# Kernel optimization log

Hardware: AMD Instinct MI355X
Metric: run time of the kernel (lower is better)

The kernel has to match this reference:

```python
import jax, jax.numpy as jnp
import numpy as np

N = 10000      # num_nodes (also input feature width per GCNConv(num_nodes, 200))
E = 320000     # num edges (avg degree 32)
H1 = 200
C = 8
N_TEST = 2000


def _gcn_norm(edge_index, edge_weight, num_nodes):
    """PyG GCNConv symmetric normalization with self-loops (fill value 1)."""
    loop = jnp.arange(num_nodes)
    row = jnp.concatenate([edge_index[0], loop])          # source nodes
    col = jnp.concatenate([edge_index[1], loop])          # target nodes
    w = jnp.concatenate([edge_weight, jnp.ones((num_nodes,), edge_weight.dtype)])
    deg = jax.ops.segment_sum(w, col, num_segments=num_nodes)
    dis = jnp.where(deg > 0, jax.lax.rsqrt(deg), 0.0)     # deg^{-1/2}, 0 for isolated
    norm = dis[row] * w * dis[col]
    return row, col, norm


def _gcn_conv(x, row, col, norm, W, b, num_nodes):
    h = x @ W                                             # linear transform first (PyG order)
    msg = h[row] * norm[:, None]                          # gather + scale
    out = jax.ops.segment_sum(msg, col, num_segments=num_nodes)  # scatter-add aggregate
    return out + b


def setup_inputs() -> dict:
    key = jax.random.key(0)
    ks = jax.random.split(key, 8)
    x = jax.random.normal(ks[0], (N, N), jnp.float32)
    edge_index = jax.random.randint(ks[1], (2, E), 0, N, dtype=jnp.int64) if jax.config.read('jax_enable_x64') else jax.random.randint(ks[1], (2, E), 0, N)
    edge_weight = jax.random.uniform(ks[2], (E,), jnp.float32)
    mask_idx = jax.random.randint(ks[3], (N_TEST,), 0, N)
    y = jax.random.randint(ks[4], (N,), 0, C)
    W1 = jax.random.normal(ks[5], (N, H1), jnp.float32) / np.sqrt(N).astype(np.float32)
    b1 = jnp.zeros((H1,), jnp.float32)
    W2 = jax.random.normal(ks[6], (H1, C), jnp.float32) / np.sqrt(H1).astype(np.float32)
    b2 = jnp.zeros((C,), jnp.float32)
    return {"x": x, "edge_index": edge_index, "edge_weight": edge_weight,
            "mask_idx": mask_idx, "y": y, "W1": W1, "b1": b1, "W2": W2, "b2": b2}


def reference(x, edge_index, edge_weight, mask_idx, y, W1, b1, W2, b2):
    row, col, norm = _gcn_norm(edge_index, edge_weight, N)
    h = _gcn_conv(x, row, col, norm, W1, b1, N)
    h = jax.nn.relu(h)
    # dropout: module run in eval mode -> identity
    h = _gcn_conv(h, row, col, norm, W2, b2, N)
    predictions = h[mask_idx]   # masked gather (mode='test')
    targets = y[mask_idx]
    return predictions, targets
```

## Files before the change

kernel.cpp:

```cpp
#include <hip/hip_runtime.h>
#include <hip/hip_bf16.h>

#define NN     10000
#define NE     320000
#define H1DIM  200
#define H1BST  208
#define NCLS   8
#define NTST   2000
#define KDIM   10000
#define KPAD   10048
#define KSPL   6
#define KSTEPS 26
#define NGEMMB 474

typedef __bf16 bf16x8 __attribute__((ext_vector_type(8)));
typedef float  f32x4  __attribute__((ext_vector_type(4)));

__device__ __forceinline__ void load_lds16(const void* g, void* l) {
  __builtin_amdgcn_global_load_lds(
      (__attribute__((address_space(1))) void*)(void*)g,
      (__attribute__((address_space(3))) void*)l, 16, 0, 0);
}


__global__ void k_prep0(float* deg, int* cnt, int* cur, int* flags,
                        const unsigned* ei, const unsigned* mk, const unsigned* yy,
                        const float* __restrict__ W1, __bf16* __restrict__ Wt) {
  __shared__ float tile[64][65];
  __shared__ int s_f[4];
  int b = blockIdx.x, t = threadIdx.x;
  if (b < 40) {
    int i = b * 256 + t;
    if (i < NN) { deg[i] = 1.0f; cnt[i] = 0; cur[i] = 0; }
    return;
  }
  if (b < 43) {
    unsigned a = 0;
    if (b == 40)      { for (int i = t; i < 2048; i += 256) a |= ei[2 * i + 1]; }
    else if (b == 41) { for (int i = t; i < 2048; i += 256) a |= yy[2 * i + 1]; }
    else              { for (int i = t; i < 900;  i += 256) a |= mk[2 * i + 1]; }
    int wid = t >> 6;
    int any = __any(a != 0) ? 1 : 0;
    if ((t & 63) == 0) s_f[wid] = any;
    __syncthreads();
    if (t == 0) {
      int f = s_f[0] | s_f[1] | s_f[2] | s_f[3];
      int idx = (b == 40) ? 0 : (b == 41) ? 2 : 1;
      flags[idx] = f;
    }
    return;
  }
  int bt = b - 43;
  int k0 = (bt % 157) * 64, n0 = (bt / 157) * 64;
  int tn = t & 63, tk = t >> 6;
  for (int r = 0; r < 64; r += 4) {
    int k = k0 + tk + r, n = n0 + tn;
    tile[tk + r][tn] = (k < KDIM && n < H1DIM) ? W1[k * H1DIM + n] : 0.f;
  }
  __syncthreads();
  for (int r = 0; r < 64; r += 4) {
    int n = n0 + tk + r, k = k0 + tn;
    if (k < KPAD && n < 256)
      Wt[(size_t)n * KPAD + k] = (__bf16)tile[tn][tk + r];
  }
}


__launch_bounds__(512, 4)
__global__ void k_gemm_cvt(const float* __restrict__ x, const __bf16* __restrict__ Wt,
                           __bf16* __restrict__ hpart,
                           const void* ei, const void* mk, const void* yy,
                           const float* __restrict__ ew, const int* __restrict__ flags,
                           int* idx32, int* mask32, int* y32, float* deg, int* cnt) {
  int t = threadIdx.x;
  if (blockIdx.x >= NGEMMB) {
    int i = (blockIdx.x - NGEMMB) * 512 + t;
    if (i < NE) {
      int v = (flags[0] == 0) ? (int)((const long long*)ei)[i] : ((const int*)ei)[i];
      idx32[i] = min(max(v, 0), NN - 1);
    } else if (i < 2 * NE) {
      int v = (flags[0] == 0) ? (int)((const long long*)ei)[i] : ((const int*)ei)[i];
      v = min(max(v, 0), NN - 1);
      idx32[i] = v;
      atomicAdd(&deg[v], ew[i - NE]);
      atomicAdd(&cnt[v], 1);
    } else if (i < 2 * NE + NTST) {
      int j = i - 2 * NE;
      int v = (flags[1] == 0) ? (int)((const long long*)mk)[j] : ((const int*)mk)[j];
      mask32[j] = min(max(v, 0), NN - 1);
    } else if (i < 2 * NE + NTST + NN) {
      int j = i - 2 * NE - NTST;
      int v = (flags[2] == 0) ? (int)((const long long*)yy)[j] : ((const int*)yy)[j];
      y32[j] = min(max(v, 0), NN - 1);
    }
    return;
  }

  __shared__ __align__(16) __bf16 As[128 * 64];
  __shared__ __align__(16) __bf16 Bs[256 * 64];
  int wv = t >> 6, lane = t & 63;
  int wm = wv >> 2, wn = wv & 3;
  int m0 = (blockIdx.x % 79) * 128;
  int split = blockIdx.x / 79;
  int kbeg = split * (KSTEPS * 64);
  int nsteps = KSTEPS + ((split == KSPL - 1) ? 1 : 0);

  f32x4 acc[4][4];
  #pragma unroll
  for (int i = 0; i < 4; ++i)
    #pragma unroll
    for (int j = 0; j < 4; ++j)
      #pragma unroll
      for (int r = 0; r < 4; ++r) acc[i][j][r] = 0.f;

  int am = t >> 2;
  int ac = t & 3;
  long arow = m0 + am; if (arow >= NN) arow = NN - 1;
  const float* aptr = x + (size_t)arow * KDIM + ac * 16;
  int ag0 = (2 * ac + 0) ^ (am & 7);
  int ag1 = (2 * ac + 1) ^ (am & 7);
  __bf16* awr0 = As + am * 64 + ag0 * 8;
  __bf16* awr1 = As + am * 64 + ag1 * 8;

  const __bf16* bsrc[4];
  __bf16* bdst[4];
  #pragma unroll
  for (int pass = 0; pass < 4; ++pass) {
    int s = pass * 512 + t;
    int brow = s >> 3, bg = s & 7;
    bsrc[pass] = Wt + (size_t)brow * KPAD + ((bg ^ (brow & 7)) * 8);
    bdst[pass] = Bs + (size_t)(pass * 512 + wv * 64) * 8;
  }

  int lrow = lane & 15;
  int lhi = lane >> 4;
  int lx7 = lane & 7;

  float4 v0, v1, v2, v3;
  {
    bool pr = (kbeg + ac * 16 + 16 <= KDIM);
    if (pr) {
      const float4* p = (const float4*)(aptr + kbeg);
      v0 = p[0]; v1 = p[1]; v2 = p[2]; v3 = p[3];
    }
  }

  for (int ks = 0; ks < nsteps; ++ks) {
    int k0 = kbeg + ks * 64;
    #pragma unroll
    for (int pass = 0; pass < 4; ++pass)
      load_lds16(bsrc[pass] + k0, bdst[pass]);
    {
      bool pr = (k0 + ac * 16 + 16 <= KDIM);
      bf16x8 bva, bvb;
      if (pr) {
        bva[0] = (__bf16)v0.x; bva[1] = (__bf16)v0.y;
        bva[2] = (__bf16)v0.z; bva[3] = (__bf16)v0.w;
        bva[4] = (__bf16)v1.x; bva[5] = (__bf16)v1.y;
        bva[6] = (__bf16)v1.z; bva[7] = (__bf16)v1.w;
        bvb[0] = (__bf16)v2.x; bvb[1] = (__bf16)v2.y;
        bvb[2] = (__bf16)v2.z; bvb[3] = (__bf16)v2.w;
        bvb[4] = (__bf16)v3.x; bvb[5] = (__bf16)v3.y;
        bvb[6] = (__bf16)v3.z; bvb[7] = (__bf16)v3.w;
      } else {
        #pragma unroll
        for (int q = 0; q < 8; ++q) { bva[q] = (__bf16)0.f; bvb[q] = (__bf16)0.f; }
      }
      *(bf16x8*)awr0 = bva;
      *(bf16x8*)awr1 = bvb;
    }
    __syncthreads();

    if (ks + 1 < nsteps) {
      int k1 = k0 + 64;
      bool pr = (k1 + ac * 16 + 16 <= KDIM);
      if (pr) {
        const float4* p = (const float4*)(aptr + k1);
        v0 = p[0]; v1 = p[1]; v2 = p[2]; v3 = p[3];
      }
    }

    #pragma unroll
    for (int kk = 0; kk < 2; ++kk) {
      int gs8 = ((kk * 4 + lhi) ^ lx7) * 8;
      bf16x8 af[4], bf[4];
      #pragma unroll
      for (int i = 0; i < 4; ++i)
        af[i] = *(const bf16x8*)&As[(wm * 64 + i * 16 + lrow) * 64 + gs8];
      #pragma unroll
      for (int j = 0; j < 4; ++j)
        bf[j] = *(const bf16x8*)&Bs[(wn * 64 + j * 16 + lrow) * 64 + gs8];
      #pragma unroll
      for (int i = 0; i < 4; ++i)
        #pragma unroll
        for (int j = 0; j < 4; ++j)
          acc[i][j] = __builtin_amdgcn_mfma_f32_16x16x32_bf16(af[i], bf[j], acc[i][j], 0, 0, 0);
    }
    __syncthreads();
  }

  __bf16* outp = hpart + (size_t)split * NN * H1BST;
  int colb = wn * 64 + (lane & 15);
  int rbase = m0 + wm * 64 + ((lane >> 4) * 4);
  #pragma unroll
  for (int i = 0; i < 4; ++i)
    #pragma unroll
    for (int j = 0; j < 4; ++j) {
      int cg = colb + j * 16;
      if (cg < H1BST) {
        #pragma unroll
        for (int r = 0; r < 4; ++r) {
          int rg = rbase + i * 16 + r;
          if (rg < NN) outp[(size_t)rg * H1BST + cg] = (__bf16)acc[i][j][r];
        }
      }
    }
}


__global__ void k_scan_red(const int* __restrict__ cnt, const float* __restrict__ deg,
                           float* dis, int* rowptr,
                           const __bf16* __restrict__ hpart, __bf16* __restrict__ h1b) {
  int t = threadIdx.x;
  if (blockIdx.x > 0) {
    int i = (blockIdx.x - 1) * 1024 + t;
    if (i < NN * 26) {
      int c = i / 26, ch = i - c * 26;
      size_t base = (size_t)c * H1BST + ch * 8;
      float s[8];
      #pragma unroll
      for (int q = 0; q < 8; ++q) s[q] = 0.f;
      #pragma unroll
      for (int sp = 0; sp < KSPL; ++sp) {
        bf16x8 v = *(const bf16x8*)(hpart + (size_t)sp * NN * H1BST + base);
        #pragma unroll
        for (int q = 0; q < 8; ++q) s[q] += (float)v[q];
      }
      bf16x8 o;
      #pragma unroll
      for (int q = 0; q < 8; ++q) o[q] = (__bf16)s[q];
      *(bf16x8*)&h1b[base] = o;
    }
    return;
  }
  __shared__ int wsum[16];
  __shared__ int carry;
  int lane = t & 63, wid = t >> 6;
  if (t == 0) carry = 0;
  __syncthreads();
  for (int base = 0; base < NN; base += 1024) {
    int idx = base + t;
    if (idx < NN) { float d = deg[idx]; dis[idx] = (d > 0.f) ? rsqrtf(d) : 0.f; }
    int v = (idx < NN) ? cnt[idx] : 0;
    int x = v;
    #pragma unroll
    for (int off = 1; off < 64; off <<= 1) {
      int y = __shfl_up(x, off);
      if (lane >= off) x += y;
    }
    if (lane == 63) wsum[wid] = x;
    __syncthreads();
    int c0 = carry;
    if (t < 16) {
      int s = wsum[t];
      #pragma unroll
      for (int off = 1; off < 16; off <<= 1) {
        int y = __shfl_up(s, off);
        if (t >= off) s += y;
      }
      wsum[t] = s;
    }
    __syncthreads();
    int woff = (wid == 0) ? 0 : wsum[wid - 1];
    if (idx < NN) rowptr[idx] = c0 + woff + x - v;
    int tot = wsum[15];
    __syncthreads();
    if (t == 0) carry = c0 + tot;
    __syncthreads();
  }
  if (t == 0) rowptr[NN] = carry;
}

__global__ void k_norm_scatter(const int* __restrict__ rows, const int* __restrict__ cols,
                               const float* __restrict__ w, const float* __restrict__ dis,
                               const int* __restrict__ rowptr, int* cur,
                               float* normv, int* eids) {
  int e = blockIdx.x * 512 + threadIdx.x;
  if (e < NE) {
    int r = rows[e], c = cols[e];
    normv[e] = dis[r] * w[e] * dis[c];
    int pos = rowptr[c] + atomicAdd(&cur[c], 1);
    eids[pos] = e;
  }
}


__global__ void k_agg1lin2(const __bf16* __restrict__ h1b, const float* __restrict__ dis,
                           const float* __restrict__ normv, const int* __restrict__ rows,
                           const int* __restrict__ rowptr, const int* __restrict__ eids,
                           const float* __restrict__ b1, const float* __restrict__ W2,
                           float* __restrict__ h2) {
  __shared__ int   s_r[512];
  __shared__ float s_n[512];
  __shared__ float s_p[4][8];
  int c = blockIdx.x;
  int t = threadIdx.x;
  int lane = t & 63, wid = t >> 6;
  int p0 = rowptr[c], len = rowptr[c + 1] - p0;
  float acc = 0.f;
  for (int base = 0; base < len; base += 512) {
    int chunk = min(512, len - base);
    for (int j = t; j < chunk; j += 256) {
      int e = eids[p0 + base + j];
      s_r[j] = rows[e];
      s_n[j] = normv[e];
    }
    __syncthreads();
    if (t < H1DIM) {
      int j = 0;
      for (; j + 4 <= chunk; j += 4) {
        float v0 = s_n[j + 0] * (float)h1b[(size_t)s_r[j + 0] * H1BST + t];
        float v1 = s_n[j + 1] * (float)h1b[(size_t)s_r[j + 1] * H1BST + t];
        float v2 = s_n[j + 2] * (float)h1b[(size_t)s_r[j + 2] * H1BST + t];
        float v3 = s_n[j + 3] * (float)h1b[(size_t)s_r[j + 3] * H1BST + t];
        acc += v0 + v1 + v2 + v3;
      }
      for (; j < chunk; ++j) acc += s_n[j] * (float)h1b[(size_t)s_r[j] * H1BST + t];
    }
    __syncthreads();
  }
  float a = 0.f;
  if (t < H1DIM) {
    float d = dis[c];
    a = acc + d * d * (float)h1b[(size_t)c * H1BST + t] + b1[t];
    a = fmaxf(a, 0.f);
  }
  float p[8];
  if (t < H1DIM) {
    float4 w2a = *(const float4*)&W2[t * 8];
    float4 w2b = *(const float4*)&W2[t * 8 + 4];
    p[0] = a * w2a.x; p[1] = a * w2a.y; p[2] = a * w2a.z; p[3] = a * w2a.w;
    p[4] = a * w2b.x; p[5] = a * w2b.y; p[6] = a * w2b.z; p[7] = a * w2b.w;
  } else {
    #pragma unroll
    for (int o = 0; o < 8; ++o) p[o] = 0.f;
  }
  #pragma unroll
  for (int s = 32; s >= 1; s >>= 1) {
    #pragma unroll
    for (int o = 0; o < 8; ++o) p[o] += __shfl_down(p[o], s);
  }
  if (lane == 0) {
    #pragma unroll
    for (int o = 0; o < 8; ++o) s_p[wid][o] = p[o];
  }
  __syncthreads();
  if (t < 8)
    h2[(size_t)c * 8 + t] = s_p[0][t] + s_p[1][t] + s_p[2][t] + s_p[3][t];
}


__global__ void k_agg2out(const float* __restrict__ h2, const float* __restrict__ dis,
                          const float* __restrict__ normv, const int* __restrict__ rows,
                          const int* __restrict__ rowptr, const int* __restrict__ eids,
                          const float* __restrict__ b2, const int* __restrict__ mask,
                          const int* __restrict__ yv, float* __restrict__ out) {
  int i = blockIdx.x * 256 + threadIdx.x;
  if (i < NTST * NCLS) {
    int r = i >> 3, o = i & 7;
    int c = mask[r];
    float d = dis[c];
    float acc = d * d * h2[c * NCLS + o];
    int p0 = rowptr[c], p1 = rowptr[c + 1];
    for (int j = p0; j < p1; ++j) {
      int e = eids[j];
      acc += normv[e] * h2[rows[e] * NCLS + o];
    }
    out[i] = acc + b2[o];
  } else if (i < NTST * NCLS + NTST) {
    int r = i - NTST * NCLS;
    out[i] = (float)yv[mask[r]];
  }
}


extern "C" void kernel_launch(void* const* d_in, const int* in_sizes, int n_in,
                              void* d_out, int out_size, void* d_ws, size_t ws_size,
                              hipStream_t stream) {
  const float* x    = (const float*)d_in[0];
  const void*  ei   = d_in[1];
  const float* ew   = (const float*)d_in[2];
  const void*  mask = d_in[3];
  const void*  y    = d_in[4];
  const float* W1   = (const float*)d_in[5];
  const float* b1   = (const float*)d_in[6];
  const float* W2   = (const float*)d_in[7];
  const float* b2   = (const float*)d_in[8];
  float* out = (float*)d_out;

  char* ws = (char*)d_ws;
  float* deg    = (float*)(ws + 0);
  float* dis    = (float*)(ws + (64 << 10));
  float* normv  = (float*)(ws + (128 << 10));
  int*   idx32  = (int*)(ws + (2 << 20));
  float* h2     = (float*)(ws + (5 << 20));
  int*   mask32 = (int*)(ws + (6 << 20));
  int*   y32    = (int*)(ws + (6 << 20) + (64 << 10));
  int*   flags  = (int*)(ws + (6 << 20) + (128 << 10));
  int*   cnt    = (int*)(ws + (6 << 20) + (256 << 10));
  int*   cur    = (int*)(ws + (6 << 20) + (384 << 10));
  int*   rowptr = (int*)(ws + (6 << 20) + (512 << 10));
  int*   eids   = (int*)(ws + (7 << 20));
  __bf16* Wt    = (__bf16*)(ws + ((size_t)9 << 20));
  __bf16* h1b   = (__bf16*)(ws + ((size_t)16 << 20));
  __bf16* hpart = (__bf16*)(ws + ((size_t)24 << 20));

  int* rows32 = idx32;
  int* cols32 = idx32 + NE;

  k_prep0<<<dim3(671), dim3(256), 0, stream>>>(deg, cnt, cur, flags,
                                               (const unsigned*)ei, (const unsigned*)mask,
                                               (const unsigned*)y, W1, Wt);

  k_gemm_cvt<<<dim3(NGEMMB + 1274), dim3(512), 0, stream>>>(
      x, Wt, hpart, ei, mask, y, ew, flags, idx32, mask32, y32, deg, cnt);

  k_scan_red<<<dim3(255), dim3(1024), 0, stream>>>(cnt, deg, dis, rowptr, hpart, h1b);

  k_norm_scatter<<<dim3(625), dim3(512), 0, stream>>>(rows32, cols32, ew, dis, rowptr, cur,
                                                      normv, eids);

  k_agg1lin2<<<dim3(10000), dim3(256), 0, stream>>>(h1b, dis, normv, rows32, rowptr, eids,
                                                    b1, W2, h2);
  k_agg2out<<<dim3(71), dim3(256), 0, stream>>>(h2, dis, normv, rows32, rowptr, eids, b2,
                                                mask32, y32, out);
}
```

Measured before the change: 255.2 us.

## Vectorize layer-1 aggregation with 16-byte bf16 loads split across edge groups

Restructures the per-node aggregation kernel so each thread loads 8 bf16 features at once (16-byte vector loads) and the 256 threads are split into 8 edge groups of 32 lanes, each handling a strided subset of neighbors. Partial sums are reduced across edge groups through shared memory, and the second-layer linear projection is then done per 8-feature chunk with a shared-memory final sum. This cuts the number of scalar 2-byte gathers and uses all threads instead of 200. In exchange it needs more shared memory, extra reduction passes and barriers, and 6 of every 32 lanes sit idle.

New measurement: 251.9 us. About the same (-1.3%).

```diff
diff --git a/kernel.cpp b/kernel.cpp
--- a/kernel.cpp
+++ b/kernel.cpp
@@ -302,12 +302,17 @@
                            float* __restrict__ h2) {
   __shared__ int   s_r[512];
   __shared__ float s_n[512];
-  __shared__ float s_p[4][8];
+  __shared__ float s_acc[8][26][8];
+  __shared__ float s_p[26][8];
   int c = blockIdx.x;
   int t = threadIdx.x;
-  int lane = t & 63, wid = t >> 6;
+  int es = t >> 5;
+  int f8 = t & 31;
+  float acc8[8];
+  #pragma unroll
+  for (int q = 0; q < 8; ++q) acc8[q] = 0.f;
+
   int p0 = rowptr[c], len = rowptr[c + 1] - p0;
-  float acc = 0.f;
   for (int base = 0; base < len; base += 512) {
     int chunk = min(512, len - base);
     for (int j = t; j < chunk; j += 256) {
@@ -316,47 +321,67 @@
       s_n[j] = normv[e];
     }
     __syncthreads();
-    if (t < H1DIM) {
-      int j = 0;
-      for (; j + 4 <= chunk; j += 4) {
-        float v0 = s_n[j + 0] * (float)h1b[(size_t)s_r[j + 0] * H1BST + t];
-        float v1 = s_n[j + 1] * (float)h1b[(size_t)s_r[j + 1] * H1BST + t];
-        float v2 = s_n[j + 2] * (float)h1b[(size_t)s_r[j + 2] * H1BST + t];
-        float v3 = s_n[j + 3] * (float)h1b[(size_t)s_r[j + 3] * H1BST + t];
-        acc += v0 + v1 + v2 + v3;
-      }
-      for (; j < chunk; ++j) acc += s_n[j] * (float)h1b[(size_t)s_r[j] * H1BST + t];
-    }
-    __syncthreads();
-  }
-  float a = 0.f;
-  if (t < H1DIM) {
+    if (f8 < 26) {
+      for (int j = es; j < chunk; j += 8) {
+        float nv = s_n[j];
+        bf16x8 v = *(const bf16x8*)&h1b[(size_t)s_r[j] * H1BST + f8 * 8];
+        #pragma unroll
+        for (int q = 0; q < 8; ++q) acc8[q] += nv * (float)v[q];
+      }
+    }
+    __syncthreads();
+  }
+
+  if (f8 < 26) {
+    #pragma unroll
+    for (int q = 0; q < 8; ++q) s_acc[es][f8][q] = acc8[q];
+  }
+  __syncthreads();
+
+  if (es == 0 && f8 < 26) {
+    bf16x8 selfv = *(const bf16x8*)&h1b[(size_t)c * H1BST + f8 * 8];
     float d = dis[c];
-    a = acc + d * d * (float)h1b[(size_t)c * H1BST + t] + b1[t];
-    a = fmaxf(a, 0.f);
-  }
-  float p[8];
-  if (t < H1DIM) {
-    float4 w2a = *(const float4*)&W2[t * 8];
-    float4 w2b = *(const float4*)&W2[t * 8 + 4];
-    p[0] = a * w2a.x; p[1] = a * w2a.y; p[2] = a * w2a.z; p[3] = a * w2a.w;
-    p[4] = a * w2b.x; p[5] = a * w2b.y; p[6] = a * w2b.z; p[7] = a * w2b.w;
-  } else {
+    float dd = d * d;
+    float a[8];
+    #pragma unroll
+    for (int q = 0; q < 8; ++q) {
+      float s = 0.f;
+      #pragma unroll
+      for (int e2 = 0; e2 < 8; ++e2) s += s_acc[e2][f8][q];
+      int feat = f8 * 8 + q;
+      if (feat < H1DIM) {
+        float av = s + dd * (float)selfv[q] + b1[feat];
+        a[q] = fmaxf(av, 0.f);
+      } else {
+        a[q] = 0.f;
+      }
+    }
+    float p[8];
     #pragma unroll
     for (int o = 0; o < 8; ++o) p[o] = 0.f;
-  }
-  #pragma unroll
-  for (int s = 32; s >= 1; s >>= 1) {
-    #pragma unroll
-    for (int o = 0; o < 8; ++o) p[o] += __shfl_down(p[o], s);
-  }
-  if (lane == 0) {
-    #pragma unroll
-    for (int o = 0; o < 8; ++o) s_p[wid][o] = p[o];
+    #pragma unroll
+    for (int q = 0; q < 8; ++q) {
+      int feat = f8 * 8 + q;
+      if (feat < H1DIM) {
+        float4 wa = *(const float4*)&W2[feat * 8];
+        float4 wb = *(const float4*)&W2[feat * 8 + 4];
+        p[0] += a[q] * wa.x; p[1] += a[q] * wa.y;
+        p[2] += a[q] * wa.z; p[3] += a[q] * wa.w;
+        p[4] += a[q] * wb.x; p[5] += a[q] * wb.y;
+        p[6] += a[q] * wb.z; p[7] += a[q] * wb.w;
+      }
+    }
+    #pragma unroll
+    for (int o = 0; o < 8; ++o) s_p[f8][o] = p[o];
   }
   __syncthreads();
-  if (t < 8)
-    h2[(size_t)c * 8 + t] = s_p[0][t] + s_p[1][t] + s_p[2][t] + s_p[3][t];
+
+  if (t < 8) {
+    float s = 0.f;
+    #pragma unroll
+    for (int q = 0; q < 26; ++q) s += s_p[q][t];
+    h2[(size_t)c * 8 + t] = s;
+  }
 }
 
 
```
